# Optimization experiments

Hardware: AMD Instinct MI355X
Metric: run time of the kernel (lower is better)

The kernel has to match this reference:

```python
import jax, jax.numpy as jnp
import numpy as np


def setup_inputs() -> dict:
    key = jax.random.key(0)
    k0, k1, k2, k3 = jax.random.split(key, 4)
    B, H, W, C, h = 2, 64, 64, 256, 8
    N = H * W
    # per-pixel, per-head (dy, dx) match offsets; a few pixels of displacement
    max_offset = jax.random.normal(k0, (B, N, h, 2), dtype=jnp.float32) * 4.0
    q = jax.random.normal(k1, (B, N, C), dtype=jnp.float32)
    k = jax.random.normal(k2, (B, N, C), dtype=jnp.float32)
    v = jax.random.normal(k3, (B, N, C), dtype=jnp.float32)
    return {"max_offset": max_offset, "q": q, "k": k, "v": v,
            "H": H, "W": W, "r_h": 3, "r_w": 3}


def reference(max_offset, q, k, v, H, W, r_h, r_w):
    """MatchAttention fused forward (l1_norm, scale=1.0).

    Each query pixel (y,x), head g attends to a (2*r_h+1)x(2*r_w+1) window
    centered at (y,x) + round(max_offset[...,g]), clamped to the image.
    Similarity is the negative L1 distance between q and gathered k.
    Returns (output [B,N,C], attn_out [B,N,h,K]).
    """
    B, N, C = q.shape
    h = max_offset.shape[2]
    Ch = C // h
    scale = 1.0
    attn_type = "l1_norm"  # fixed; 'l2_norm' would use squared distance

    # window deltas, K = (2*r_h+1)*(2*r_w+1)
    dy = jnp.arange(-r_h, r_h + 1)
    dx = jnp.arange(-r_w, r_w + 1)
    gy, gx = jnp.meshgrid(dy, dx, indexing="ij")
    ddy, ddx = gy.reshape(-1), gx.reshape(-1)  # [K]

    ys = (jnp.arange(N) // W)[None, :, None]  # [1,N,1]
    xs = (jnp.arange(N) % W)[None, :, None]

    off = jnp.round(max_offset).astype(jnp.int32)  # [B,N,h,2] (dy,dx)
    cy = ys + off[..., 0]                          # [B,N,h] window center
    cx = xs + off[..., 1]
    py = jnp.clip(cy[..., None] + ddy, 0, H - 1)   # [B,N,h,K]
    px = jnp.clip(cx[..., None] + ddx, 0, W - 1)
    idx = py * W + px                              # flat pixel index, [B,N,h,K]

    # split heads and move head axis forward: [B,h,N,Ch]
    qh = q.reshape(B, N, h, Ch).transpose(0, 2, 1, 3)
    kh = k.reshape(B, N, h, Ch).transpose(0, 2, 1, 3)
    vh = v.reshape(B, N, h, Ch).transpose(0, 2, 1, 3)
    idx_t = idx.transpose(0, 2, 1, 3)              # [B,h,N,K]

    # gather windows: [B,h,N,K,Ch]
    gather = jax.vmap(jax.vmap(lambda tbl, i: tbl[i]))
    kg = gather(kh, idx_t)
    vg = gather(vh, idx_t)

    # negative L1 distance similarity, softmax over window
    sim = -scale * jnp.abs(qh[:, :, :, None, :] - kg).sum(-1)  # [B,h,N,K]
    attn = jax.nn.softmax(sim, axis=-1)

    out = jnp.einsum("bhnk,bhnkc->bhnc", attn, vg)
    output = out.transpose(0, 2, 1, 3).reshape(B, N, C)
    attn_out = attn.transpose(0, 2, 1, 3)          # [B,N,h,K]
    return output, attn_out
```

## Files before the change

kernel.cpp:

```cpp
#include <hip/hip_runtime.h>
#include <hip/hip_fp16.h>
#include <math.h>

constexpr int B = 2, H = 64, W = 64, C = 256, NH = 8, CH = 32;
constexpr int R = 3, KW = 7, KK = 49, N = H * W;
constexpr int PIX = 32;

template <int CTRL>
static __device__ __forceinline__ float dpp_mov(float v) {
  union { float f; int i; } u;
  u.f = v;
  u.i = __builtin_amdgcn_update_dpp(u.i, u.i, CTRL, 0xf, 0xf, true);
  return u.f;
}
#define DPP_QUAD_XOR1 0xB1
#define DPP_QUAD_XOR2 0x4E
#define DPP_HALF_MIRROR 0x141

__global__ void __launch_bounds__(256) pack_kv_kernel(
    const float* __restrict__ kp, const float* __restrict__ vp,
    __half* __restrict__ kv) {
  const int idx = blockIdx.x * 256 + threadIdx.x;
  const int e8 = idx & 7;
  const int g = (idx >> 3) & 7;
  const int bn = idx >> 6;
  const float4 kf = *(const float4*)(kp + (size_t)bn * C + g * CH + e8 * 4);
  const float4 vf = *(const float4*)(vp + (size_t)bn * C + g * CH + e8 * 4);
  __half2 o[4];
  o[0] = __floats2half2_rn(kf.x, kf.y);
  o[1] = __floats2half2_rn(kf.z, kf.w);
  o[2] = __floats2half2_rn(vf.x, vf.y);
  o[3] = __floats2half2_rn(vf.z, vf.w);
  *(float4*)(kv + ((size_t)(bn * NH + g) * 64 + e8 * 8)) = *(float4*)o;
}

union KV { float4 f; __half2 h[4]; };

__global__ void __launch_bounds__(256, 2) match_attn_kernel(
    const float* __restrict__ moff, const float* __restrict__ qp,
    const __half* __restrict__ kvp, float* __restrict__ outp,
    float* __restrict__ attnp) {
  const int t = threadIdx.x;
  const int e8 = t & 7;
  const int p = t >> 3;

  const int xcd = blockIdx.x & 7;
  const int rest = blockIdx.x >> 3;
  const int bg = xcd * 2 + (rest >> 7);
  const int slot = rest & 127;
  const int y = slot >> 1;
  const int x = (slot & 1) * PIX + p;
  const int g = bg & 7;
  const int b = bg >> 3;
  const int n = y * W + x;

  const float2 off = *(const float2*)(moff + ((size_t)(b * N + n) * NH + g) * 2);
  const int cy = y + (int)rintf(off.x);
  const int cx = x + (int)rintf(off.y);

  int pxo[KW];
#pragma unroll
  for (int i = 0; i < KW; ++i) pxo[i] = min(max(cx + i - R, 0), W - 1) << 10;
  const char* kvimg = (const char*)kvp +
      (size_t)b * N * NH * 128 + g * 128 + e8 * 16;

  const int chn = g * CH + e8 * 4;
  const float4 q0 = *(const float4*)(qp + (size_t)(b * N + n) * C + chn);
  const __half2 q01 = __floats2half2_rn(q0.x, q0.y);
  const __half2 q23 = __floats2half2_rn(q0.z, q0.w);

  float ev7[KW];
#pragma unroll
  for (int i = 0; i < KW; ++i) ev7[i] = 0.f;
  float4 acc = {0.f, 0.f, 0.f, 0.f};
  float d0 = 0.f, d1 = 0.f;

#define ROWOFF(iy) (min(max(cy + (iy) - R, 0), H - 1) << 16)
#define LOADROW(buf, iy)                                            \
  {                                                                 \
    const int _ro = ROWOFF(iy);                                     \
    _Pragma("unroll") for (int ix = 0; ix < KW; ++ix)               \
        buf[ix].f = *(const float4*)(kvimg + (_ro + pxo[ix]));      \
  }
#define COMPROW(buf, iy)                                            \
  {                                                                 \
    const bool _own = ((iy) == e8);                                 \
    _Pragma("unroll") for (int ix = 0; ix < KW; ++ix) {             \
      const __half2 d01h = __habs2(__hsub2(q01, buf[ix].h[0]));     \
      const __half2 d23h = __habs2(__hsub2(q23, buf[ix].h[1]));     \
      const float2 f01 = __half22float2(d01h);                      \
      const float2 f23 = __half22float2(d23h);                      \
      float s = (f01.x + f01.y) + (f23.x + f23.y);                  \
      s += dpp_mov<DPP_QUAD_XOR1>(s);                               \
      s += dpp_mov<DPP_QUAD_XOR2>(s);                               \
      s += dpp_mov<DPP_HALF_MIRROR>(s);                             \
      const float e = __expf(-s);  \
      if (ix & 1) d1 += e; else d0 += e;                            \
      if (_own) ev7[ix] = e;                                        \
      const float2 v01 = __half22float2(buf[ix].h[2]);              \
      const float2 v23 = __half22float2(buf[ix].h[3]);              \
      acc.x += e * v01.x; acc.y += e * v01.y;                       \
      acc.z += e * v23.x; acc.w += e * v23.y;                       \
    }                                                               \
  }

  KV A[KW], Bf[KW];
  LOADROW(A, 0)
#pragma clang loop unroll(disable)
  for (int ty = 0; ty < KW - 1; ty += 2) {
    LOADROW(Bf, ty + 1)
    COMPROW(A, ty)
    LOADROW(A, ty + 2)
    COMPROW(Bf, ty + 1)
  }
  COMPROW(A, KW - 1)

  const float inv = 1.0f / (d0 + d1);
  float4 o;
  o.x = acc.x * inv; o.y = acc.y * inv; o.z = acc.z * inv; o.w = acc.w * inv;
  *(float4*)(outp + (size_t)(b * N + n) * C + chn) = o;

  if (e8 < KW) {
    float* attn_row = attnp + ((size_t)(b * N + n) * NH + g) * KK + e8 * KW;
#pragma unroll
    for (int ix = 0; ix < KW; ++ix) attn_row[ix] = ev7[ix] * inv;
  }
}

extern "C" void kernel_launch(void* const* d_in, const int* in_sizes, int n_in,
                              void* d_out, int out_size, void* d_ws, size_t ws_size,
                              hipStream_t stream) {
  const float* moff = (const float*)d_in[0];
  const float* q    = (const float*)d_in[1];
  const float* k    = (const float*)d_in[2];
  const float* v    = (const float*)d_in[3];
  float* out  = (float*)d_out;
  float* attn = out + (size_t)B * N * C;
  __half* kv = (__half*)d_ws;

  pack_kv_kernel<<<B * N * NH * 8 / 256, 256, 0, stream>>>(k, v, kv);
  const int grid = B * NH * N / PIX;
  match_attn_kernel<<<grid, 256, 0, stream>>>(moff, q, kv, out, attn);
}
```

Baseline: 112.8 us.

## Split K and V halves across lane pairs with 16 lanes per pixel

Each pixel now uses 16 lanes instead of 8. Even lanes load the K half of the packed fp16 record and odd lanes load the V half, each with 8-byte loads instead of 16-byte loads. The L1 sum adds a row-mirror DPP step and zeroes the contribution of V lanes. The grid doubles to 16 pixels per block. The aim is more thread-level parallelism and lower per-thread register and load pressure, at the cost of duplicated exp and softmax work and half the lanes idling on each half of the math.

```diff
diff --git a/kernel.cpp b/kernel.cpp
--- a/kernel.cpp
+++ b/kernel.cpp
@@ -4,7 +4,6 @@
 
 constexpr int B = 2, H = 64, W = 64, C = 256, NH = 8, CH = 32;
 constexpr int R = 3, KW = 7, KK = 49, N = H * W;
-constexpr int PIX = 32;
 
 template <int CTRL>
 static __device__ __forceinline__ float dpp_mov(float v) {
@@ -16,6 +15,7 @@
 #define DPP_QUAD_XOR1 0xB1
 #define DPP_QUAD_XOR2 0x4E
 #define DPP_HALF_MIRROR 0x141
+#define DPP_ROW_MIRROR 0x140
 
 __global__ void __launch_bounds__(256) pack_kv_kernel(
     const float* __restrict__ kp, const float* __restrict__ vp,
@@ -34,22 +34,24 @@
   *(float4*)(kv + ((size_t)(bn * NH + g) * 64 + e8 * 8)) = *(float4*)o;
 }
 
-union KV { float4 f; __half2 h[4]; };
+union KV8 { float2 f; __half2 h[2]; };
 
 __global__ void __launch_bounds__(256, 2) match_attn_kernel(
     const float* __restrict__ moff, const float* __restrict__ qp,
     const __half* __restrict__ kvp, float* __restrict__ outp,
     float* __restrict__ attnp) {
   const int t = threadIdx.x;
-  const int e8 = t & 7;
-  const int p = t >> 3;
+  const int e16 = t & 15;
+  const int p = t >> 4;
+  const bool klane = !(e16 & 1);
+  const int chunk = e16 >> 1;
 
   const int xcd = blockIdx.x & 7;
   const int rest = blockIdx.x >> 3;
-  const int bg = xcd * 2 + (rest >> 7);
-  const int slot = rest & 127;
-  const int y = slot >> 1;
-  const int x = (slot & 1) * PIX + p;
+  const int bg = xcd * 2 + (rest >> 8);
+  const int slot = rest & 255;
+  const int y = slot >> 2;
+  const int x = (slot & 3) * 16 + p;
   const int g = bg & 7;
   const int b = bg >> 3;
   const int n = y * W + x;
@@ -62,9 +64,9 @@
 #pragma unroll
   for (int i = 0; i < KW; ++i) pxo[i] = min(max(cx + i - R, 0), W - 1) << 10;
   const char* kvimg = (const char*)kvp +
-      (size_t)b * N * NH * 128 + g * 128 + e8 * 16;
+      (size_t)b * N * NH * 128 + g * 128 + e16 * 8;
 
-  const int chn = g * CH + e8 * 4;
+  const int chn = g * CH + chunk * 4;
   const float4 q0 = *(const float4*)(qp + (size_t)(b * N + n) * C + chn);
   const __half2 q01 = __floats2half2_rn(q0.x, q0.y);
   const __half2 q23 = __floats2half2_rn(q0.z, q0.w);
@@ -80,31 +82,33 @@
   {                                                                 \
     const int _ro = ROWOFF(iy);                                     \
     _Pragma("unroll") for (int ix = 0; ix < KW; ++ix)               \
-        buf[ix].f = *(const float4*)(kvimg + (_ro + pxo[ix]));      \
+        buf[ix].f = *(const float2*)(kvimg + (_ro + pxo[ix]));      \
   }
 #define COMPROW(buf, iy)                                            \
   {                                                                 \
-    const bool _own = ((iy) == e8);                                 \
+    const bool _own = ((iy) == e16);                                \
     _Pragma("unroll") for (int ix = 0; ix < KW; ++ix) {             \
-      const __half2 d01h = __habs2(__hsub2(q01, buf[ix].h[0]));     \
-      const __half2 d23h = __habs2(__hsub2(q23, buf[ix].h[1]));     \
-      const float2 f01 = __half22float2(d01h);                      \
-      const float2 f23 = __half22float2(d23h);                      \
+      const __half2 a01 = __habs2(__hsub2(q01, buf[ix].h[0]));      \
+      const __half2 a23 = __habs2(__hsub2(q23, buf[ix].h[1]));      \
+      const float2 f01 = __half22float2(a01);                       \
+      const float2 f23 = __half22float2(a23);                       \
       float s = (f01.x + f01.y) + (f23.x + f23.y);                  \
+      if (!klane) s = 0.f;  \
       s += dpp_mov<DPP_QUAD_XOR1>(s);                               \
       s += dpp_mov<DPP_QUAD_XOR2>(s);                               \
       s += dpp_mov<DPP_HALF_MIRROR>(s);                             \
+      s += dpp_mov<DPP_ROW_MIRROR>(s);                              \
       const float e = __expf(-s);  \
       if (ix & 1) d1 += e; else d0 += e;                            \
       if (_own) ev7[ix] = e;                                        \
-      const float2 v01 = __half22float2(buf[ix].h[2]);              \
-      const float2 v23 = __half22float2(buf[ix].h[3]);              \
-      acc.x += e * v01.x; acc.y += e * v01.y;                       \
-      acc.z += e * v23.x; acc.w += e * v23.y;                       \
+      const float2 v01 = __half22float2(buf[ix].h[0]);              \
+      const float2 v23 = __half22float2(buf[ix].h[1]);              \
+      acc.x += e * v01.x; acc.y += e * v01.y;   \
+      acc.z += e * v23.x; acc.w += e * v23.y;   \
     }                                                               \
   }
 
-  KV A[KW], Bf[KW];
+  KV8 A[KW], Bf[KW];
   LOADROW(A, 0)
 #pragma clang loop unroll(disable)
   for (int ty = 0; ty < KW - 1; ty += 2) {
@@ -116,12 +120,14 @@
   COMPROW(A, KW - 1)
 
   const float inv = 1.0f / (d0 + d1);
-  float4 o;
-  o.x = acc.x * inv; o.y = acc.y * inv; o.z = acc.z * inv; o.w = acc.w * inv;
-  *(float4*)(outp + (size_t)(b * N + n) * C + chn) = o;
-
-  if (e8 < KW) {
-    float* attn_row = attnp + ((size_t)(b * N + n) * NH + g) * KK + e8 * KW;
+  if (!klane) {
+    float4 o;
+    o.x = acc.x * inv; o.y = acc.y * inv;
+    o.z = acc.z * inv; o.w = acc.w * inv;
+    *(float4*)(outp + (size_t)(b * N + n) * C + chn) = o;
+  }
+  if (e16 < KW) {
+    float* attn_row = attnp + ((size_t)(b * N + n) * NH + g) * KK + e16 * KW;
 #pragma unroll
     for (int ix = 0; ix < KW; ++ix) attn_row[ix] = ev7[ix] * inv;
   }
@@ -139,6 +145,6 @@
   __half* kv = (__half*)d_ws;
 
   pack_kv_kernel<<<B * N * NH * 8 / 256, 256, 0, stream>>>(k, v, kv);
-  const int grid = B * NH * N / PIX;
+  const int grid = B * NH * N / 16;
   match_attn_kernel<<<grid, 256, 0, stream>>>(moff, q, kv, out, attn);
 }
```

Result: slower. 129.0 us (+14.4%).
